# Kernel tuning notes

Measured on AMD Instinct MI355X. Metric: run time of the kernel, lower is better.

## Reference

```python
import jax, jax.numpy as jnp
import numpy as np

N, H, B, E = 8192, 64, 8, 262144


def setup_inputs() -> dict:
    key = jax.random.key(0)
    ks = jax.random.split(key, 16)
    inp = {
        "x": jax.random.uniform(ks[0], (B, N, 2), dtype=jnp.float32),
        "edge_index": jax.random.randint(ks[1], (2, E), 0, N, dtype=jnp.int64),
        "target_node": jax.random.randint(ks[2], (B,), 0, N, dtype=jnp.int64),
        "current_prereq_mask": jax.random.uniform(ks[3], (B, N), dtype=jnp.float32),
        # learned parameters (eval mode: dropout is identity)
        "node_emb": jax.random.normal(ks[4], (N, H), dtype=jnp.float32) * 0.02,
        "W_sp": jax.random.normal(ks[5], (H, 2), dtype=jnp.float32) * 0.5,
        "b_sp": jnp.zeros((H,), dtype=jnp.float32),
        "W_g": jax.random.normal(ks[6], (H, H), dtype=jnp.float32) * (1.0 / np.sqrt(H)),
        "b_g": jnp.zeros((H,), dtype=jnp.float32),
        "W_d": jax.random.normal(ks[7], (1, H), dtype=jnp.float32) * (1.0 / np.sqrt(H)),
        "b_d": jnp.zeros((1,), dtype=jnp.float32),
        "W_a": jax.random.normal(ks[8], (1, H), dtype=jnp.float32) * (1.0 / np.sqrt(H)),
        "b_a": jnp.zeros((1,), dtype=jnp.float32),
        "prereq_w": jnp.array([1.0], dtype=jnp.float32),
    }
    return inp


def _build_adj_norm(edge_index):
    # A_hat = A + I ; adj_norm = D^{-1/2} A_hat D^{-1/2}, dense [N, N]
    adj = jnp.zeros((N, N), dtype=jnp.float32).at[edge_index[0], edge_index[1]].set(1.0)
    adj = adj + jnp.eye(N, dtype=jnp.float32)
    deg = adj.sum(axis=1)
    dis = jnp.where(deg > 0, deg ** -0.5, 0.0)
    return dis[:, None] * adj * dis[None, :]


def reference(x, edge_index, target_node, current_prereq_mask,
              node_emb, W_sp, b_sp, W_g, b_g, W_d, b_d, W_a, b_a, prereq_w):
    adj_norm = _build_adj_norm(edge_index)               # [N, N]
    h = node_emb[None] + x @ W_sp.T + b_sp               # [B, N, H]
    h_proj = h @ W_g.T                                   # [B, N, H]
    z = jnp.einsum('nm,bmh->bnh', adj_norm, h_proj) + b_g
    z = jax.nn.relu(z)                                   # [B, N, H]

    target_emb = jnp.take_along_axis(z, target_node[:, None, None].astype(jnp.int32).repeat(1, axis=1), axis=1)[:, 0, :]  # [B, H]
    difficulty = (target_emb @ W_d.T + b_d)[:, 0]        # [B]

    scores = x[:, :, 1]                                  # [B, N]
    n_learned = jnp.clip(x[:, :, 0].sum(axis=1), 1.0)    # [B]
    weighted_z = jnp.einsum('bnh,bn->bh', z, scores) / n_learned[:, None]
    ability = (weighted_z @ W_a.T + b_a)[:, 0]           # [B]

    z_pos = jax.nn.softplus(z)
    prereq_agg = jnp.einsum('bnh,bn->bh', z_pos, current_prereq_mask).mean(axis=-1)  # [B]
    prereq_strength = jnp.abs(prereq_w)[0] * prereq_agg

    gap = ability - difficulty + prereq_strength
    prob = jax.nn.sigmoid(gap)
    return prob, gap
```

## Files before the change

kernel.cpp:

```cpp
#include <hip/hip_runtime.h>
#include <hip/hip_fp16.h>
#include <math.h>

#define N 8192
#define H 64
#define B 8
#define MAXDEG 128
#define REPS 8

#define OFF_CNT  0ULL
#define OFF_WR   32768ULL
#define OFF_PR   49152ULL
#define OFF_NLR  65536ULL
#define ZERO_END 65792ULL
#define OFF_COLS 65792ULL
#define OFF_TGT  2162944ULL
#define OFF_UV   2164992ULL
#define OFF_REC  2165760ULL

__global__ __launch_bounds__(256) void k_zero(float4* __restrict__ p) {
    unsigned i = blockIdx.x * 256u + threadIdx.x;
    if (i < (unsigned)(ZERO_END / 16))
        p[i] = make_float4(0.f, 0.f, 0.f, 0.f);
}

__global__ __launch_bounds__(256) void k_edges(const int* __restrict__ ei, int nE,
                                               unsigned* __restrict__ cnt,
                                               unsigned short* __restrict__ cols) {
    int e = blockIdx.x * 256 + threadIdx.x;
    if (e >= nE) return;
    int r = ei[e];
    int c = ei[nE + e];
    unsigned k = atomicAdd(&cnt[r], 1u);
    if (k < MAXDEG) cols[r * MAXDEG + k] = (unsigned short)c;
}

__global__ __launch_bounds__(256) void k_prep(const float* __restrict__ ne,
                                              const float* __restrict__ W_g,
                                              const float* __restrict__ W_sp,
                                              const float* __restrict__ b_sp,
                                              const float* __restrict__ x,
                                              const float* __restrict__ pmask,
                                              unsigned* __restrict__ cnt,
                                              unsigned short* __restrict__ cols,
                                              unsigned* __restrict__ rec,
                                              float* __restrict__ uvec) {
    __shared__ float wgs[H * 65];
    __shared__ unsigned short ls[4][MAXDEG];
    const int tid = threadIdx.x, lane = tid & 63, wv = tid >> 6;
    const int bid = blockIdx.x;

    for (int e = tid; e < H * H; e += 256)
        wgs[(e >> 6) * 65 + (e & 63)] = W_g[e];
    __syncthreads();

    float wr[H];
#pragma unroll
    for (int k = 0; k < H; ++k) wr[k] = wgs[lane * 65 + k];

    if (bid == 0 && wv == 0) {
        float v0 = W_sp[lane * 2 + 0], v1 = W_sp[lane * 2 + 1], vb = b_sp[lane];
        float a0 = 0.f, a1 = 0.f, a2 = 0.f;
#pragma unroll
        for (int k = 0; k < H; ++k) {
            a0 = fmaf(wr[k], __shfl(v0, k, 64), a0);
            a1 = fmaf(wr[k], __shfl(v1, k, 64), a1);
            a2 = fmaf(wr[k], __shfl(vb, k, 64), a2);
        }
        uvec[lane] = a0; uvec[64 + lane] = a1; uvec[128 + lane] = a2;
    }

    for (int i = 0; i < 2; ++i) {
        const int r = (bid * 4 + wv) * 2 + i;
        const int kraw = min((int)cnt[r], MAXDEG);
        unsigned short* cl = &cols[r * MAXDEG];
        for (int t = lane; t < kraw; t += 64) ls[wv][t] = cl[t];
        int c0 = (lane < kraw) ? (int)ls[wv][lane] : -1;
        int dup0 = 0;
        for (int j = 0; j < lane && j < kraw; ++j)
            dup0 |= ((int)ls[wv][j] == c0);
        unsigned long long m0 = __ballot((lane < kraw) && !dup0);
        unsigned long long below = (1ULL << lane) - 1ULL;
        unsigned tot = __popcll(m0);
        if ((lane < kraw) && !dup0)
            cl[__popcll(m0 & below)] = (unsigned short)c0;
        if (kraw > 64) {
            const int i1 = lane + 64;
            int c1 = (i1 < kraw) ? (int)ls[wv][i1] : -2;
            int dup1 = 0;
            for (int j = 0; j < i1 && j < kraw; ++j)
                dup1 |= ((int)ls[wv][j] == c1);
            unsigned long long m1 = __ballot((i1 < kraw) && !dup1);
            if ((i1 < kraw) && !dup1)
                cl[tot + __popcll(m1 & below)] = (unsigned short)c1;
            tot += __popcll(m1);
        }
        if (lane == 0) cnt[r] = tot;
        const float dis = rsqrtf((float)(tot + 1u));

        float xvx = 0.f, xvy = 0.f, pm = 0.f;
        if (lane < 8) {
            float2 t2 = ((const float2*)x)[lane * N + r];
            xvx = t2.x; xvy = t2.y;
        }
        if (lane >= 17 && lane < 25) pm = pmask[(lane - 17) * N + r];
        float yv = __shfl(xvy, lane & 7, 64);
        float aux = (lane < 8)   ? dis * xvx
                  : (lane < 16)  ? dis * yv
                  : (lane == 16) ? dis
                  : (lane < 25)  ? pm : 0.f;

        const float4* ne4 = (const float4*)(ne + (size_t)r * H);
        float acc = 0.f;
#pragma unroll
        for (int kk = 0; kk < 16; ++kk) {
            float4 h4 = ne4[kk];
            acc = fmaf(wr[4 * kk + 0], h4.x, acc);
            acc = fmaf(wr[4 * kk + 1], h4.y, acc);
            acc = fmaf(wr[4 * kk + 2], h4.z, acc);
            acc = fmaf(wr[4 * kk + 3], h4.w, acc);
        }
        unsigned w = ((unsigned)__half_as_ushort(__float2half(dis * acc)) << 16)
                   |  (unsigned)__half_as_ushort(__float2half(aux));
        rec[(size_t)r * 64 + lane] = w;
    }
}

__global__ __launch_bounds__(1024, 2) void k_spmm(const unsigned* __restrict__ rec,
                                                  const unsigned* __restrict__ cnt,
                                                  const unsigned short* __restrict__ cols,
                                                  const float* __restrict__ uvec,
                                                  const float* __restrict__ b_g,
                                                  const int* __restrict__ target,
                                                  float* __restrict__ wr_,
                                                  float* __restrict__ pr_,
                                                  float* __restrict__ nlr,
                                                  float* __restrict__ tgt) {
    __shared__ float lw[B * H];
    __shared__ float lp[B * H];
    __shared__ float lnl[B];
    const int tid = threadIdx.x;
    const int lane = tid & 63, wv = tid >> 6;
    const int r = blockIdx.x * 16 + wv;

    if (tid < B * H) { lw[tid] = 0.f; lp[tid] = 0.f; }
    if (tid < B) lnl[tid] = 0.f;
    __syncthreads();

    const float u0 = uvec[lane], u1 = uvec[64 + lane], ub = uvec[128 + lane];
    const float bg = b_g[lane];
    int tg[B];
#pragma unroll
    for (int b = 0; b < B; ++b) tg[b] = target[b];

    const unsigned vown = rec[(size_t)r * 64 + lane];
    float2 fown = __half22float2(*(const __half2*)&vown);

    const int kc = min((int)cnt[r], MAXDEG);
    const unsigned short* cl = &cols[r * MAXDEG];
    int creg = (lane < kc) ? (int)cl[lane] : 0;

    float spA = fown.y, sxA = fown.x, spB = 0.f, sxB = 0.f;
    const int kc64 = min(kc, 64);
    int k = 0;
    for (; k + 2 <= kc64; k += 2) {
        int cA = __shfl(creg, k, 64);
        int cB = __shfl(creg, k + 1, 64);
        unsigned vA = rec[(size_t)cA * 64 + lane];
        unsigned vB = rec[(size_t)cB * 64 + lane];
        float2 fA = __half22float2(*(const __half2*)&vA);
        float2 fB = __half22float2(*(const __half2*)&vB);
        spA += fA.y; sxA += fA.x;
        spB += fB.y; sxB += fB.x;
    }
    if (k < kc64) {
        int c = __shfl(creg, k, 64);
        unsigned v = rec[(size_t)c * 64 + lane];
        float2 f = __half22float2(*(const __half2*)&v);
        spA += f.y; sxA += f.x;
    }
    for (int kk = 64; kk < kc; ++kk) {
        int c = (int)cl[kk];
        unsigned v = rec[(size_t)c * 64 + lane];
        float2 f = __half22float2(*(const __half2*)&v);
        spA += f.y; sxA += f.x;
    }
    const float sp = spA + spB;
    const float sx = sxA + sxB;

    const float dis_r = __shfl(fown.x, 16, 64);
    const float rdis = 1.0f / dis_r;
    const float sd = __shfl(sx, 16, 64);
    const float base = fmaf(sd, ub, sp);
#pragma unroll
    for (int b = 0; b < B; ++b) {
        float sx0 = __shfl(sx, b, 64);
        float sx1 = __shfl(sx, 8 + b, 64);
        float sc  = __shfl(fown.x, 8 + b, 64) * rdis;
        float mk  = __shfl(fown.x, 17 + b, 64);
        float v = fmaf(sx0, u0, fmaf(sx1, u1, base));
        float z = fmaxf(fmaf(dis_r, v, bg), 0.f);
        atomicAdd(&lw[b * H + lane], z * sc);
        atomicAdd(&lp[b * H + lane], (z + __logf(1.f + __expf(-z))) * mk);
        if (r == tg[b]) tgt[b * H + lane] = z;
    }
    if (lane < 8) atomicAdd(&lnl[lane], fown.x * rdis);
    __syncthreads();

    const int rep = blockIdx.x & (REPS - 1);
    if (tid < B * H)           atomicAdd(&wr_[rep * B * H + tid], lw[tid]);
    else if (tid < 2 * B * H)  atomicAdd(&pr_[rep * B * H + tid - B * H], lp[tid - B * H]);
    if (tid < B)               atomicAdd(&nlr[rep * B + tid], lnl[tid]);
}

__global__ __launch_bounds__(512) void k_final(const float* __restrict__ wr_,
                                               const float* __restrict__ pr_,
                                               const float* __restrict__ nlr,
                                               const float* __restrict__ tgt,
                                               const float* __restrict__ W_d,
                                               const float* __restrict__ b_d,
                                               const float* __restrict__ W_a,
                                               const float* __restrict__ b_a,
                                               const float* __restrict__ prereq_w,
                                               float* __restrict__ out) {
    int tid = threadIdx.x, b = tid >> 6, h = tid & 63;
    float ws = 0.f, ps = 0.f, nlv = 0.f;
#pragma unroll
    for (int rep = 0; rep < REPS; ++rep) {
        ws  += wr_[(rep * B + b) * H + h];
        ps  += pr_[(rep * B + b) * H + h];
        nlv += nlr[rep * B + b];
    }
    float nl = fmaxf(nlv, 1.0f);
    float ap = (ws / nl) * W_a[h];
    float dp = tgt[b * H + h] * W_d[h];
    float pp = ps;
    for (int off = 32; off; off >>= 1) {
        ap += __shfl_down(ap, off, 64);
        dp += __shfl_down(dp, off, 64);
        pp += __shfl_down(pp, off, 64);
    }
    if (h == 0) {
        float ability    = ap + b_a[0];
        float difficulty = dp + b_d[0];
        float preq       = fabsf(prereq_w[0]) * (pp * (1.0f / (float)H));
        float gap  = ability - difficulty + preq;
        float prob = 1.0f / (1.0f + __expf(-gap));
        out[b]     = prob;
        out[B + b] = gap;
    }
}

extern "C" void kernel_launch(void* const* d_in, const int* in_sizes, int n_in,
                              void* d_out, int out_size, void* d_ws, size_t ws_size,
                              hipStream_t stream) {
    const float* x        = (const float*)d_in[0];
    const int*   ei       = (const int*)d_in[1];
    const int*   target   = (const int*)d_in[2];
    const float* pmask    = (const float*)d_in[3];
    const float* ne       = (const float*)d_in[4];
    const float* W_sp     = (const float*)d_in[5];
    const float* b_sp     = (const float*)d_in[6];
    const float* W_g      = (const float*)d_in[7];
    const float* b_g      = (const float*)d_in[8];
    const float* W_d      = (const float*)d_in[9];
    const float* b_d      = (const float*)d_in[10];
    const float* W_a      = (const float*)d_in[11];
    const float* b_a      = (const float*)d_in[12];
    const float* prereq_w = (const float*)d_in[13];

    const int nE = in_sizes[1] / 2;

    char* ws = (char*)d_ws;
    unsigned*        cnt  = (unsigned*)(ws + OFF_CNT);
    float*           wr_  = (float*)(ws + OFF_WR);
    float*           pr_  = (float*)(ws + OFF_PR);
    float*           nlr  = (float*)(ws + OFF_NLR);
    unsigned short*  cols = (unsigned short*)(ws + OFF_COLS);
    float*           tgt  = (float*)(ws + OFF_TGT);
    float*           uvec = (float*)(ws + OFF_UV);
    unsigned*        rec  = (unsigned*)(ws + OFF_REC);

    k_zero<<<(unsigned)(ZERO_END / 16 + 255) / 256, 256, 0, stream>>>((float4*)ws);
    k_edges<<<(nE + 255) / 256, 256, 0, stream>>>(ei, nE, cnt, cols);
    k_prep<<<N / 8, 256, 0, stream>>>(ne, W_g, W_sp, b_sp, x, pmask, cnt, cols,
                                      rec, uvec);
    k_spmm<<<N / 16, 1024, 0, stream>>>(rec, cnt, cols, uvec, b_g, target,
                                        wr_, pr_, nlr, tgt);
    k_final<<<1, 512, 0, stream>>>(wr_, pr_, nlr, tgt, W_d, b_d, W_a, b_a,
                                   prereq_w, (float*)d_out);
}
```

Baseline: 89.92 us.

## Process four rows per wavefront in SpMM with interleaved neighbor gathers

Each wavefront now handles four adjacent rows instead of one, interleaving the four rows' neighbor gathers in one loop so more independent loads are in flight per wave. Column indices are read directly from global memory per step instead of being broadcast via shuffles. Blocks shrink to 256 threads with higher occupancy hints, and the shared-memory reduction cost is spread over more rows per block. The risks are fewer waves overall, load imbalance when the four rows have different degrees, and uncoalesced per-step column-index loads.

```diff
diff --git a/kernel.cpp b/kernel.cpp
--- a/kernel.cpp
+++ b/kernel.cpp
@@ -126,24 +126,30 @@
     }
 }
 
-__global__ __launch_bounds__(1024, 2) void k_spmm(const unsigned* __restrict__ rec,
-                                                  const unsigned* __restrict__ cnt,
-                                                  const unsigned short* __restrict__ cols,
-                                                  const float* __restrict__ uvec,
-                                                  const float* __restrict__ b_g,
-                                                  const int* __restrict__ target,
-                                                  float* __restrict__ wr_,
-                                                  float* __restrict__ pr_,
-                                                  float* __restrict__ nlr,
-                                                  float* __restrict__ tgt) {
+__device__ __forceinline__ void acc_u32(unsigned u, float& p, float& a) {
+    float2 f = __half22float2(*(const __half2*)&u);
+    p += f.y; a += f.x;
+}
+
+__global__ __launch_bounds__(256, 8) void k_spmm(const unsigned* __restrict__ rec,
+                                                 const unsigned* __restrict__ cnt,
+                                                 const unsigned short* __restrict__ cols,
+                                                 const float* __restrict__ uvec,
+                                                 const float* __restrict__ b_g,
+                                                 const int* __restrict__ target,
+                                                 float* __restrict__ wr_,
+                                                 float* __restrict__ pr_,
+                                                 float* __restrict__ nlr,
+                                                 float* __restrict__ tgt) {
     __shared__ float lw[B * H];
     __shared__ float lp[B * H];
     __shared__ float lnl[B];
     const int tid = threadIdx.x;
     const int lane = tid & 63, wv = tid >> 6;
-    const int r = blockIdx.x * 16 + wv;
-
-    if (tid < B * H) { lw[tid] = 0.f; lp[tid] = 0.f; }
+    const int wid = blockIdx.x * 4 + wv;
+
+    lw[tid] = 0.f; lw[tid + 256] = 0.f;
+    lp[tid] = 0.f; lp[tid + 256] = 0.f;
     if (tid < B) lnl[tid] = 0.f;
     __syncthreads();
 
@@ -153,64 +159,63 @@
 #pragma unroll
     for (int b = 0; b < B; ++b) tg[b] = target[b];
 
-    const unsigned vown = rec[(size_t)r * 64 + lane];
-    float2 fown = __half22float2(*(const __half2*)&vown);
-
-    const int kc = min((int)cnt[r], MAXDEG);
-    const unsigned short* cl = &cols[r * MAXDEG];
-    int creg = (lane < kc) ? (int)cl[lane] : 0;
-
-    float spA = fown.y, sxA = fown.x, spB = 0.f, sxB = 0.f;
-    const int kc64 = min(kc, 64);
-    int k = 0;
-    for (; k + 2 <= kc64; k += 2) {
-        int cA = __shfl(creg, k, 64);
-        int cB = __shfl(creg, k + 1, 64);
-        unsigned vA = rec[(size_t)cA * 64 + lane];
-        unsigned vB = rec[(size_t)cB * 64 + lane];
-        float2 fA = __half22float2(*(const __half2*)&vA);
-        float2 fB = __half22float2(*(const __half2*)&vB);
-        spA += fA.y; sxA += fA.x;
-        spB += fB.y; sxB += fB.x;
-    }
-    if (k < kc64) {
-        int c = __shfl(creg, k, 64);
-        unsigned v = rec[(size_t)c * 64 + lane];
+    int   r_[4], kc_[4];
+    float sp_[4], sx_[4], fx_[4];
+    const unsigned short* cl_[4];
+#pragma unroll
+    for (int i = 0; i < 4; ++i) {
+        const int r = wid * 4 + i;
+        r_[i] = r;
+        kc_[i] = min((int)cnt[r], MAXDEG);
+        cl_[i] = &cols[r * MAXDEG];
+        unsigned v = rec[(size_t)r * 64 + lane];
         float2 f = __half22float2(*(const __half2*)&v);
-        spA += f.y; sxA += f.x;
-    }
-    for (int kk = 64; kk < kc; ++kk) {
-        int c = (int)cl[kk];
-        unsigned v = rec[(size_t)c * 64 + lane];
-        float2 f = __half22float2(*(const __half2*)&v);
-        spA += f.y; sxA += f.x;
-    }
-    const float sp = spA + spB;
-    const float sx = sxA + sxB;
-
-    const float dis_r = __shfl(fown.x, 16, 64);
-    const float rdis = 1.0f / dis_r;
-    const float sd = __shfl(sx, 16, 64);
-    const float base = fmaf(sd, ub, sp);
-#pragma unroll
-    for (int b = 0; b < B; ++b) {
-        float sx0 = __shfl(sx, b, 64);
-        float sx1 = __shfl(sx, 8 + b, 64);
-        float sc  = __shfl(fown.x, 8 + b, 64) * rdis;
-        float mk  = __shfl(fown.x, 17 + b, 64);
-        float v = fmaf(sx0, u0, fmaf(sx1, u1, base));
-        float z = fmaxf(fmaf(dis_r, v, bg), 0.f);
-        atomicAdd(&lw[b * H + lane], z * sc);
-        atomicAdd(&lp[b * H + lane], (z + __logf(1.f + __expf(-z))) * mk);
-        if (r == tg[b]) tgt[b * H + lane] = z;
-    }
-    if (lane < 8) atomicAdd(&lnl[lane], fown.x * rdis);
+        sp_[i] = f.y;
+        sx_[i] = f.x;
+        fx_[i] = f.x;
+    }
+    const int kmax = max(max(kc_[0], kc_[1]), max(kc_[2], kc_[3]));
+    for (int k = 0; k < kmax; ++k) {
+        unsigned v0 = 0u, v1 = 0u, v2 = 0u, v3 = 0u;
+        if (k < kc_[0]) v0 = rec[(size_t)cl_[0][k] * 64 + lane];
+        if (k < kc_[1]) v1 = rec[(size_t)cl_[1][k] * 64 + lane];
+        if (k < kc_[2]) v2 = rec[(size_t)cl_[2][k] * 64 + lane];
+        if (k < kc_[3]) v3 = rec[(size_t)cl_[3][k] * 64 + lane];
+        acc_u32(v0, sp_[0], sx_[0]);
+        acc_u32(v1, sp_[1], sx_[1]);
+        acc_u32(v2, sp_[2], sx_[2]);
+        acc_u32(v3, sp_[3], sx_[3]);
+    }
+
+#pragma unroll
+    for (int i = 0; i < 4; ++i) {
+        const float sp = sp_[i], sx = sx_[i];
+        const float dis_r = __shfl(fx_[i], 16, 64);
+        const float rdis = 1.0f / dis_r;
+        const float sd = __shfl(sx, 16, 64);
+        const float base = fmaf(sd, ub, sp);
+#pragma unroll
+        for (int b = 0; b < B; ++b) {
+            float sx0 = __shfl(sx, b, 64);
+            float sx1 = __shfl(sx, 8 + b, 64);
+            float sc  = __shfl(fx_[i], 8 + b, 64) * rdis;
+            float mk  = __shfl(fx_[i], 17 + b, 64);
+            float v = fmaf(sx0, u0, fmaf(sx1, u1, base));
+            float z = fmaxf(fmaf(dis_r, v, bg), 0.f);
+            atomicAdd(&lw[b * H + lane], z * sc);
+            atomicAdd(&lp[b * H + lane], (z + __logf(1.f + __expf(-z))) * mk);
+            if (r_[i] == tg[b]) tgt[b * H + lane] = z;
+        }
+        if (lane < 8) atomicAdd(&lnl[lane], fx_[i] * rdis);
+    }
     __syncthreads();
 
     const int rep = blockIdx.x & (REPS - 1);
-    if (tid < B * H)           atomicAdd(&wr_[rep * B * H + tid], lw[tid]);
-    else if (tid < 2 * B * H)  atomicAdd(&pr_[rep * B * H + tid - B * H], lp[tid - B * H]);
-    if (tid < B)               atomicAdd(&nlr[rep * B + tid], lnl[tid]);
+    atomicAdd(&wr_[rep * B * H + tid],       lw[tid]);
+    atomicAdd(&wr_[rep * B * H + tid + 256], lw[tid + 256]);
+    atomicAdd(&pr_[rep * B * H + tid],       lp[tid]);
+    atomicAdd(&pr_[rep * B * H + tid + 256], lp[tid + 256]);
+    if (tid < B) atomicAdd(&nlr[rep * B + tid], lnl[tid]);
 }
 
 __global__ __launch_bounds__(512) void k_final(const float* __restrict__ wr_,
@@ -285,8 +290,8 @@
     k_edges<<<(nE + 255) / 256, 256, 0, stream>>>(ei, nE, cnt, cols);
     k_prep<<<N / 8, 256, 0, stream>>>(ne, W_g, W_sp, b_sp, x, pmask, cnt, cols,
                                       rec, uvec);
-    k_spmm<<<N / 16, 1024, 0, stream>>>(rec, cnt, cols, uvec, b_g, target,
-                                        wr_, pr_, nlr, tgt);
+    k_spmm<<<N / 16, 256, 0, stream>>>(rec, cnt, cols, uvec, b_g, target,
+                                       wr_, pr_, nlr, tgt);
     k_final<<<1, 512, 0, stream>>>(wr_, pr_, nlr, tgt, W_d, b_d, W_a, b_a,
                                    prereq_w, (float*)d_out);
 }
```

Result: slower. 113.4 us (+26.1%).
